# Kernel optimization log

Hardware: AMD Instinct MI355X
Metric: run time of the kernel (lower is better)

The kernel has to match this reference:

```python
import jax, jax.numpy as jnp
import numpy as np

N_NODES = 30000
N_EDGES = 480000
N_GRAPHS = 128
D_IN = 128
D_H = 256
N_CLASSES = 60


def gcn_conv(x, src, dst, norm, W, b, num_nodes):
    # x: [N, d_in]; W: [d_out, d_in]; b: [d_out]
    h = x @ W.T                                   # [N, d_out]
    msg = h[src] * norm[:, None]                  # [E+N, d_out] gather + scale
    out = jax.ops.segment_sum(msg, dst, num_segments=num_nodes)  # scatter-add
    return out + b


def setup_inputs() -> dict:
    key = jax.random.key(0)
    ks = jax.random.split(key, 10)
    glorot = lambda k, o, i: jax.random.normal(k, (o, i), jnp.float32) * (2.0 / (o + i)) ** 0.5
    x = jax.random.normal(ks[0], (N_NODES, D_IN), jnp.float32)
    edge_index = jax.random.randint(ks[1], (2, N_EDGES), 0, N_NODES, jnp.int64)
    batch = jnp.sort(jax.random.randint(ks[2], (N_NODES,), 0, N_GRAPHS, jnp.int64))
    return {
        "x": x,
        "edge_index": edge_index,
        "batch": batch,
        "W1": glorot(ks[3], D_H, D_IN), "b1": jnp.zeros((D_H,), jnp.float32),
        "W2": glorot(ks[4], D_H, D_H),  "b2": jnp.zeros((D_H,), jnp.float32),
        "W3": glorot(ks[5], D_H, D_H),  "b3": jnp.zeros((D_H,), jnp.float32),
        "Wfc": glorot(ks[6], N_CLASSES, D_H),
        "bfc": jnp.zeros((N_CLASSES,), jnp.float32),
    }


def reference(x, edge_index, batch, W1, b1, W2, b2, W3, b3, Wfc, bfc):
    num_nodes = x.shape[0]
    # GCNConv default: add self-loops, symmetric normalization D^-1/2 A D^-1/2
    loops = jnp.arange(num_nodes, dtype=edge_index.dtype)
    src = jnp.concatenate([edge_index[0], loops])
    dst = jnp.concatenate([edge_index[1], loops])
    deg = jax.ops.segment_sum(jnp.ones_like(dst, dtype=x.dtype), dst,
                              num_segments=num_nodes)
    dinv = jnp.where(deg > 0, jax.lax.rsqrt(deg), 0.0)
    norm = dinv[src] * dinv[dst]                  # per-edge normalization

    h = jax.nn.relu(gcn_conv(x, src, dst, norm, W1, b1, num_nodes))
    h = jax.nn.relu(gcn_conv(h, src, dst, norm, W2, b2, num_nodes))
    h = jax.nn.relu(gcn_conv(h, src, dst, norm, W3, b3, num_nodes))

    # global_mean_pool over graph ids
    sums = jax.ops.segment_sum(h, batch, num_segments=N_GRAPHS)
    cnts = jax.ops.segment_sum(jnp.ones((num_nodes,), h.dtype), batch,
                               num_segments=N_GRAPHS)
    pooled = sums / jnp.maximum(cnts, 1.0)[:, None]   # [G, 256]
    return pooled @ Wfc.T + bfc                       # [G, num_classes]
```

## Files before the change

kernel.cpp:

```cpp
#include <hip/hip_runtime.h>
#include <cstdint>
#include <cstddef>

#define NN 30000
#define NE 480000
#define NG 128
#define DIN 128
#define DH 256
#define NC 60
#define CAP 64
#define P1MAX (NN * DIN / 4)

typedef _Float16 f16x8 __attribute__((ext_vector_type(8)));
typedef _Float16 half4_t __attribute__((ext_vector_type(4)));
typedef float f32x4 __attribute__((ext_vector_type(4)));

__device__ __forceinline__ void gload_lds16(const _Float16* g, _Float16* l) {
    __builtin_amdgcn_global_load_lds(
        (const __attribute__((address_space(1))) void*)g,
        (__attribute__((address_space(3))) void*)l, 16, 0, 0);
}

__global__ __launch_bounds__(256) void k_pre(const int* __restrict__ ei, int* __restrict__ cursor,
        int* __restrict__ csr_src,
        const float* __restrict__ x, _Float16* __restrict__ xh,
        const float* __restrict__ W1, const float* __restrict__ W2, const float* __restrict__ W3,
        _Float16* __restrict__ w1h, _Float16* __restrict__ w2h, _Float16* __restrict__ w3h,
        float* __restrict__ sums) {
    int i = blockIdx.x * 256 + threadIdx.x;
    if (i < NE) {
        int s = ei[i];
        int d = ei[NE + i];
        int slot = atomicAdd(&cursor[d], 1);
        if (slot < CAP) csr_src[d * CAP + slot] = s;
    }
    if (i < P1MAX) {
        float4 v = ((const float4*)x)[i];
        half4_t o;
        o[0] = (_Float16)v.x; o[1] = (_Float16)v.y;
        o[2] = (_Float16)v.z; o[3] = (_Float16)v.w;
        ((half4_t*)xh)[i] = o;
    }
    if (i < DH * DIN) w1h[i] = (_Float16)W1[i];
    if (i < DH * DH) {
        w2h[i] = (_Float16)W2[i];
        w3h[i] = (_Float16)W3[i];
    }
    if (i < NG * DH) sums[i] = 0.f;
}

template<int K>
__global__ __launch_bounds__(256) void k_agg(const _Float16* __restrict__ hin,
        _Float16* __restrict__ tout, const int* __restrict__ cnt,
        const int* __restrict__ csr_src) {
    constexpr int L = K / 8;
    constexpr int G = 64 / L;
    constexpr int B16 = 16 / G;
    constexpr int B8 = 8 / G;
    int node = blockIdx.x * 4 + (threadIdx.x >> 6);
    int lane = threadIdx.x & 63;
    int sub = lane / L;
    int off = lane % L;
    const _Float16* gbase = hin + off * 8;
    float acc[8];
    #pragma unroll
    for (int u = 0; u < 8; u++) acc[u] = 0.f;
    int deg = cnt[node];
    float dvd = rsqrtf((float)(deg + 1));
    int c = deg < CAP ? deg : CAP;
    int beg = node * CAP, end = beg + c;
    int e = beg;
    for (; e + 16 <= end; e += 16) {
        int s[B16]; float w[B16]; f16x8 r[B16];
        #pragma unroll
        for (int j = 0; j < B16; j++) s[j] = csr_src[e + j * G + sub];
        #pragma unroll
        for (int j = 0; j < B16; j++) r[j] = *(const f16x8*)(gbase + (size_t)s[j] * K);
        #pragma unroll
        for (int j = 0; j < B16; j++) w[j] = rsqrtf((float)(cnt[s[j]] + 1)) * dvd;
        #pragma unroll
        for (int j = 0; j < B16; j++)
            #pragma unroll
            for (int u = 0; u < 8; u++) acc[u] = fmaf(w[j], (float)r[j][u], acc[u]);
    }
    for (; e + 8 <= end; e += 8) {
        int s[B8]; float w[B8]; f16x8 r[B8];
        #pragma unroll
        for (int j = 0; j < B8; j++) s[j] = csr_src[e + j * G + sub];
        #pragma unroll
        for (int j = 0; j < B8; j++) r[j] = *(const f16x8*)(gbase + (size_t)s[j] * K);
        #pragma unroll
        for (int j = 0; j < B8; j++) w[j] = rsqrtf((float)(cnt[s[j]] + 1)) * dvd;
        #pragma unroll
        for (int j = 0; j < B8; j++)
            #pragma unroll
            for (int u = 0; u < 8; u++) acc[u] = fmaf(w[j], (float)r[j][u], acc[u]);
    }
    for (; e < end; e += G) {
        int idx = e + sub;
        int s0 = node; float w0 = 0.f;
        if (idx < end) { s0 = csr_src[idx]; w0 = rsqrtf((float)(cnt[s0] + 1)) * dvd; }
        f16x8 r0 = *(const f16x8*)(gbase + (size_t)s0 * K);
        #pragma unroll
        for (int u = 0; u < 8; u++) acc[u] = fmaf(w0, (float)r0[u], acc[u]);
    }
    {
        float sws = (sub == 0) ? dvd * dvd : 0.f;
        f16x8 rs = *(const f16x8*)(gbase + (size_t)node * K);
        #pragma unroll
        for (int u = 0; u < 8; u++) acc[u] = fmaf(sws, (float)rs[u], acc[u]);
    }
    #pragma unroll
    for (int u = 0; u < 8; u++) {
        float v = acc[u];
        #pragma unroll
        for (int m = L; m < 64; m <<= 1) v += __shfl_xor(v, m, 64);
        acc[u] = v;
    }
    if (sub == 0) {
        f16x8 o;
        #pragma unroll
        for (int u = 0; u < 8; u++) o[u] = (_Float16)acc[u];
        *(f16x8*)(tout + (size_t)node * K + off * 8) = o;
    }
}

template<int K, bool FUSE_POOL>
__global__ __launch_bounds__(256) void k_gemm(const _Float16* __restrict__ A,
        const _Float16* __restrict__ W, const float* __restrict__ bias,
        _Float16* __restrict__ Cb, const int* __restrict__ batch,
        float* __restrict__ sums) {
    __shared__ __align__(16) _Float16 lsA[2][64 * 32];
    __shared__ __align__(16) _Float16 lsB[2][64 * 32];
    int t = threadIdx.x;
    int bm = blockIdx.x * 64;
    int bn = blockIdx.y * 64;
    int lane = t & 63, wv = t >> 6;
    int wm = (wv & 1) * 32;
    int wn = (wv >> 1) * 32;
    int lm = lane & 15, q = lane >> 4;
    int r4 = t >> 2;
    int c4 = t & 3;
    int ra = bm + r4; if (ra >= NN) ra = NN - 1;
    int rb = bn + r4;
    const _Float16* gA = A + (size_t)ra * K + c4 * 8;
    const _Float16* gW = W + (size_t)rb * K + c4 * 8;

    f32x4 acc[2][2];
    #pragma unroll
    for (int i = 0; i < 2; i++)
        #pragma unroll
        for (int j = 0; j < 2; j++) acc[i][j] = (f32x4){0.f, 0.f, 0.f, 0.f};

    gload_lds16(gA, &lsA[0][t * 8]);
    gload_lds16(gW, &lsB[0][t * 8]);
    __syncthreads();
    int cur = 0;
    for (int k0 = 0; k0 < K; k0 += 32) {
        if (k0 + 32 < K) {
            gload_lds16(gA + k0 + 32, &lsA[cur ^ 1][t * 8]);
            gload_lds16(gW + k0 + 32, &lsB[cur ^ 1][t * 8]);
        }
        f16x8 bf[2];
        #pragma unroll
        for (int nt = 0; nt < 2; nt++)
            bf[nt] = *(const f16x8*)&lsB[cur][(wn + nt * 16 + lm) * 32 + q * 8];
        #pragma unroll
        for (int mt = 0; mt < 2; mt++) {
            f16x8 af = *(const f16x8*)&lsA[cur][(wm + mt * 16 + lm) * 32 + q * 8];
            #pragma unroll
            for (int nt = 0; nt < 2; nt++)
                acc[mt][nt] = __builtin_amdgcn_mfma_f32_16x16x32_f16(af, bf[nt], acc[mt][nt], 0, 0, 0);
        }
        __syncthreads();
        cur ^= 1;
    }
    if constexpr (!FUSE_POOL) {
        #pragma unroll
        for (int mt = 0; mt < 2; mt++) {
            #pragma unroll
            for (int nt = 0; nt < 2; nt++) {
                int col = bn + wn + nt * 16 + lm;
                float bv = bias[col];
                #pragma unroll
                for (int r = 0; r < 4; r++) {
                    int row = bm + wm + mt * 16 + q * 4 + r;
                    if (row < NN) {
                        float v = fmaxf(acc[mt][nt][r] + bv, 0.f);
                        Cb[(size_t)row * 256 + col] = (_Float16)v;
                    }
                }
            }
        }
    } else {
        int gid[8];
        #pragma unroll
        for (int mt = 0; mt < 2; mt++)
            #pragma unroll
            for (int r = 0; r < 4; r++) {
                int row = bm + wm + mt * 16 + q * 4 + r;
                gid[mt * 4 + r] = (row < NN) ? batch[row] : -1;
            }
        #pragma unroll
        for (int nt = 0; nt < 2; nt++) {
            int col = bn + wn + nt * 16 + lm;
            float bv = bias[col];
            float runsum = 0.f;
            int curg = -1;
            #pragma unroll
            for (int mt = 0; mt < 2; mt++) {
                #pragma unroll
                for (int r = 0; r < 4; r++) {
                    int g = gid[mt * 4 + r];
                    if (g >= 0) {
                        float v = fmaxf(acc[mt][nt][r] + bv, 0.f);
                        if (g != curg) {
                            if (curg >= 0) atomicAdd(&sums[curg * DH + col], runsum);
                            curg = g;
                            runsum = 0.f;
                        }
                        runsum += v;
                    }
                }
            }
            if (curg >= 0) atomicAdd(&sums[curg * DH + col], runsum);
        }
    }
}

__global__ __launch_bounds__(64) void k_fc(const float* __restrict__ sums,
        const int* __restrict__ batch, const float* __restrict__ Wfc,
        const float* __restrict__ bfc, float* __restrict__ out) {
    __shared__ float p[DH];
    int g = blockIdx.x;
    int t = threadIdx.x;
    int lo = 0, hi = NN;
    while (lo < hi) { int mid = (lo + hi) >> 1; if (batch[mid] < g) lo = mid + 1; else hi = mid; }
    int start = lo;
    hi = NN;
    while (lo < hi) { int mid = (lo + hi) >> 1; if (batch[mid] < g + 1) lo = mid + 1; else hi = mid; }
    int cnt = lo - start;
    float inv = (cnt > 0) ? 1.f / (float)cnt : 0.f;
    for (int i = t; i < DH; i += 64) p[i] = sums[g * DH + i] * inv;
    __syncthreads();
    if (t < NC) {
        float a = bfc[t];
        for (int k = 0; k < DH; k++) a = fmaf(p[k], Wfc[t * DH + k], a);
        out[g * NC + t] = a;
    }
}

extern "C" void kernel_launch(void* const* d_in, const int* in_sizes, int n_in,
                              void* d_out, int out_size, void* d_ws, size_t ws_size,
                              hipStream_t stream) {
    const float* x     = (const float*)d_in[0];
    const int*   ei    = (const int*)d_in[1];
    const int*   batch = (const int*)d_in[2];
    const float* W1 = (const float*)d_in[3];
    const float* b1 = (const float*)d_in[4];
    const float* W2 = (const float*)d_in[5];
    const float* b2 = (const float*)d_in[6];
    const float* W3 = (const float*)d_in[7];
    const float* b3 = (const float*)d_in[8];
    const float* Wfc = (const float*)d_in[9];
    const float* bfc = (const float*)d_in[10];
    float* out = (float*)d_out;

    char* wp = (char*)d_ws;
    auto alloc = [&](size_t bytes) {
        char* q = wp;
        wp += (bytes + 511) & ~(size_t)511;
        return (void*)q;
    };
    int*   cursor  = (int*)alloc((size_t)NN * 4);
    int*   csr_src = (int*)alloc((size_t)NN * CAP * 4);
    float* sums    = (float*)alloc((size_t)NG * DH * 4);
    _Float16* xh   = (_Float16*)alloc((size_t)NN * DIN * 2);
    _Float16* tb   = (_Float16*)alloc((size_t)NN * DH * 2);
    _Float16* hA   = (_Float16*)alloc((size_t)NN * DH * 2);
    _Float16* hB   = (_Float16*)alloc((size_t)NN * DH * 2);
    _Float16* w1h = (_Float16*)alloc((size_t)DH * DIN * 2);
    _Float16* w2h = (_Float16*)alloc((size_t)DH * DH * 2);
    _Float16* w3h = (_Float16*)alloc((size_t)DH * DH * 2);

    hipMemsetAsync(cursor, 0, (size_t)NN * 4, stream);

    k_pre<<<(P1MAX + 255) / 256, 256, 0, stream>>>(ei, cursor, csr_src, x, xh,
                                                   W1, W2, W3, w1h, w2h, w3h, sums);

    dim3 gg((NN + 63) / 64, 4);
    k_agg<128><<<NN / 4, 256, 0, stream>>>(xh, tb, cursor, csr_src);
    k_gemm<128, false><<<gg, 256, 0, stream>>>(tb, w1h, b1, hA, nullptr, nullptr);
    k_agg<256><<<NN / 4, 256, 0, stream>>>(hA, tb, cursor, csr_src);
    k_gemm<256, false><<<gg, 256, 0, stream>>>(tb, w2h, b2, hB, nullptr, nullptr);
    k_agg<256><<<NN / 4, 256, 0, stream>>>(hB, tb, cursor, csr_src);
    k_gemm<256, true><<<gg, 256, 0, stream>>>(tb, w3h, b3, nullptr, batch, sums);

    k_fc<<<NG, 64, 0, stream>>>(sums, batch, Wfc, bfc, out);
}
```

Baseline: 277.9 us.

## Fold aggregation tail into masked batch loop and re-layout GEMM LDS tiles

The aggregation kernel drops its scalar tail loop and lets the 8-wide batched loop run to the end, masking out-of-range edges with zero weight and a self index. This gives more loads in flight per iteration for the remainder edges. The GEMM kernel changes its LDS layout to a k-chunk-major arrangement, loads 64 K-columns per stage, and removes double buffering in favour of two barriers per stage. The aim is conflict-free LDS fragment reads and fewer barriers, at the cost of losing overlap between global loads and MFMA work.

New measurement: 288.0 us. 1.04x slower.

```diff
diff --git a/kernel.cpp b/kernel.cpp
--- a/kernel.cpp
+++ b/kernel.cpp
@@ -83,26 +83,25 @@
             #pragma unroll
             for (int u = 0; u < 8; u++) acc[u] = fmaf(w[j], (float)r[j][u], acc[u]);
     }
-    for (; e + 8 <= end; e += 8) {
+    for (; e < end; e += 8) {
         int s[B8]; float w[B8]; f16x8 r[B8];
         #pragma unroll
-        for (int j = 0; j < B8; j++) s[j] = csr_src[e + j * G + sub];
-        #pragma unroll
-        for (int j = 0; j < B8; j++) r[j] = *(const f16x8*)(gbase + (size_t)s[j] * K);
-        #pragma unroll
-        for (int j = 0; j < B8; j++) w[j] = rsqrtf((float)(cnt[s[j]] + 1)) * dvd;
+        for (int j = 0; j < B8; j++) {
+            int idx = e + j * G + sub;
+            s[j] = (idx < end) ? csr_src[idx] : node;
+        }
         #pragma unroll
         for (int j = 0; j < B8; j++)
+            r[j] = *(const f16x8*)(gbase + (size_t)s[j] * K);
+        #pragma unroll
+        for (int j = 0; j < B8; j++) {
+            int idx = e + j * G + sub;
+            w[j] = (idx < end) ? rsqrtf((float)(cnt[s[j]] + 1)) * dvd : 0.f;
+        }
+        #pragma unroll
+        for (int j = 0; j < B8; j++)
             #pragma unroll
             for (int u = 0; u < 8; u++) acc[u] = fmaf(w[j], (float)r[j][u], acc[u]);
-    }
-    for (; e < end; e += G) {
-        int idx = e + sub;
-        int s0 = node; float w0 = 0.f;
-        if (idx < end) { s0 = csr_src[idx]; w0 = rsqrtf((float)(cnt[s0] + 1)) * dvd; }
-        f16x8 r0 = *(const f16x8*)(gbase + (size_t)s0 * K);
-        #pragma unroll
-        for (int u = 0; u < 8; u++) acc[u] = fmaf(w0, (float)r0[u], acc[u]);
     }
     {
         float sws = (sub == 0) ? dvd * dvd : 0.f;
@@ -130,8 +129,8 @@
         const _Float16* __restrict__ W, const float* __restrict__ bias,
         _Float16* __restrict__ Cb, const int* __restrict__ batch,
         float* __restrict__ sums) {
-    __shared__ __align__(16) _Float16 lsA[2][64 * 32];
-    __shared__ __align__(16) _Float16 lsB[2][64 * 32];
+    __shared__ __align__(16) _Float16 lsA[8 * 64 * 8];
+    __shared__ __align__(16) _Float16 lsB[8 * 64 * 8];
     int t = threadIdx.x;
     int bm = blockIdx.x * 64;
     int bn = blockIdx.y * 64;
@@ -139,12 +138,12 @@
     int wm = (wv & 1) * 32;
     int wn = (wv >> 1) * 32;
     int lm = lane & 15, q = lane >> 4;
-    int r4 = t >> 2;
-    int c4 = t & 3;
-    int ra = bm + r4; if (ra >= NN) ra = NN - 1;
-    int rb = bn + r4;
-    const _Float16* gA = A + (size_t)ra * K + c4 * 8;
-    const _Float16* gW = W + (size_t)rb * K + c4 * 8;
+    int ra = bm + lane; if (ra >= NN) ra = NN - 1;
+    int rb = bn + lane;
+    const _Float16* gA = A + (size_t)ra * K + wv * 8;
+    const _Float16* gW = W + (size_t)rb * K + wv * 8;
+    _Float16* dA = lsA + (wv * 64 + lane) * 8;
+    _Float16* dW = lsB + (wv * 64 + lane) * 8;
 
     f32x4 acc[2][2];
     #pragma unroll
@@ -152,28 +151,28 @@
         #pragma unroll
         for (int j = 0; j < 2; j++) acc[i][j] = (f32x4){0.f, 0.f, 0.f, 0.f};
 
-    gload_lds16(gA, &lsA[0][t * 8]);
-    gload_lds16(gW, &lsB[0][t * 8]);
-    __syncthreads();
-    int cur = 0;
-    for (int k0 = 0; k0 < K; k0 += 32) {
-        if (k0 + 32 < K) {
-            gload_lds16(gA + k0 + 32, &lsA[cur ^ 1][t * 8]);
-            gload_lds16(gW + k0 + 32, &lsB[cur ^ 1][t * 8]);
-        }
-        f16x8 bf[2];
-        #pragma unroll
-        for (int nt = 0; nt < 2; nt++)
-            bf[nt] = *(const f16x8*)&lsB[cur][(wn + nt * 16 + lm) * 32 + q * 8];
-        #pragma unroll
-        for (int mt = 0; mt < 2; mt++) {
-            f16x8 af = *(const f16x8*)&lsA[cur][(wm + mt * 16 + lm) * 32 + q * 8];
+    for (int k0 = 0; k0 < K; k0 += 64) {
+        __syncthreads();
+        gload_lds16(gA + k0,      dA);
+        gload_lds16(gA + k0 + 32, dA + 2048);
+        gload_lds16(gW + k0,      dW);
+        gload_lds16(gW + k0 + 32, dW + 2048);
+        __syncthreads();
+        #pragma unroll
+        for (int kk = 0; kk < 2; kk++) {
+            f16x8 bf[2], af[2];
             #pragma unroll
             for (int nt = 0; nt < 2; nt++)
-                acc[mt][nt] = __builtin_amdgcn_mfma_f32_16x16x32_f16(af, bf[nt], acc[mt][nt], 0, 0, 0);
-        }
-        __syncthreads();
-        cur ^= 1;
+                bf[nt] = *(const f16x8*)&lsB[((kk * 4 + q) * 64 + (wn + nt * 16 + lm)) * 8];
+            #pragma unroll
+            for (int mt = 0; mt < 2; mt++)
+                af[mt] = *(const f16x8*)&lsA[((kk * 4 + q) * 64 + (wm + mt * 16 + lm)) * 8];
+            #pragma unroll
+            for (int mt = 0; mt < 2; mt++)
+                #pragma unroll
+                for (int nt = 0; nt < 2; nt++)
+                    acc[mt][nt] = __builtin_amdgcn_mfma_f32_16x16x32_f16(af[mt], bf[nt], acc[mt][nt], 0, 0, 0);
+        }
     }
     if constexpr (!FUSE_POOL) {
         #pragma unroll
```
